# Performance work log

Measured on AMD Instinct MI355X. Metric: run time of the kernel, lower is better.

## Reference

```python
import jax, jax.numpy as jnp
import numpy as np

N, D_HID, D_PROJ = 10000, 256, 256
TAU = 0.5


def setup_inputs() -> dict:
    key = jax.random.key(0)
    ks = jax.random.split(key, 7)
    s = 1.0 / np.sqrt(D_HID)
    return {
        "z1": jax.random.normal(ks[0], (N, D_HID), jnp.float32),
        "z2": jax.random.normal(ks[1], (N, D_HID), jnp.float32),
        "z3": jax.random.normal(ks[2], (N, D_HID), jnp.float32),
        "W1": jax.random.normal(ks[3], (D_PROJ, D_HID), jnp.float32) * s,
        "b1": jnp.zeros((D_PROJ,), jnp.float32),
        "W2": jax.random.normal(ks[4], (D_HID, D_PROJ), jnp.float32) * s,
        "b2": jnp.zeros((D_HID,), jnp.float32),
    }


def _projection(z, W1, b1, W2, b2):
    h = jax.nn.elu(z @ W1.T + b1)
    return h @ W2.T + b2


def _normalize(z, eps=1e-12):
    n = jnp.linalg.norm(z, axis=1, keepdims=True)
    return z / jnp.maximum(n, eps)


def _semi_loss(z1, z2, z3, tau):
    # exp of three NxN cosine-similarity matrices / tau
    intra = jnp.exp(z1 @ z1.T / tau)
    inter = jnp.exp(z1 @ z2.T / tau)
    neg = jnp.exp(z1 @ z3.T / tau)
    denom = (intra.sum(1) + inter.sum(1) + neg.sum(1)
             - jnp.diag(intra) - jnp.diag(inter) - jnp.diag(neg))
    return -jnp.log(jnp.diag(inter) / denom)


def reference(z1, z2, z3, W1, b1, W2, b2):
    p1 = _normalize(_projection(z1, W1, b1, W2, b2))
    p2 = _normalize(_projection(z2, W1, b1, W2, b2))
    p3 = _normalize(_projection(z3, W1, b1, W2, b2))
    l1 = _semi_loss(p1, p2, p3, TAU)
    l2 = _semi_loss(p2, p1, p3, TAU)
    return ((l1 + l2) * 0.5).mean()
```

## Files before the change

kernel.cpp:

```cpp
#include <hip/hip_runtime.h>
#include <hip/hip_bf16.h>
#include <hip/hip_fp8.h>
#include <math.h>

#define AS1 __attribute__((address_space(1)))
#define AS3 __attribute__((address_space(3)))

typedef __bf16 bf16x8 __attribute__((ext_vector_type(8)));
typedef __bf16 bf16x4 __attribute__((ext_vector_type(4)));
typedef float  f32x4  __attribute__((ext_vector_type(4)));
typedef long   longx2 __attribute__((ext_vector_type(2)));

static constexpr int   N_ROWS   = 10000;
static constexpr int   D        = 256;
static constexpr float INV_TAU  = 2.0f;

static constexpr int   T        = 79;
static constexpr int   NP       = T * 128;
static constexpr float PADF     = 112.0f;
static constexpr int   SPR     = 10;
static constexpr int   BPJ     = T * SPR;
static constexpr int   NWGG    = 5 * BPJ;

static constexpr int   PT       = 79;

__device__ __forceinline__ void tile_gemm_128(
    const __bf16* __restrict__ Abase, const __bf16* __restrict__ Bbase,
    char* ldsA, char* ldsB, int tid, f32x4 acc[4][4])
{
  const int l      = tid & 63;
  const int wr     = (tid >> 7) & 1;
  const int wc     = (tid >> 6) & 1;
  const int srow   = tid >> 3;
  const int schunk = tid & 7;
  const int lrow   = l & 15;
  const int lk     = l >> 4;

  for (int kt = 0; kt < 4; ++kt) {
    __syncthreads();
    const int kbase = kt * 64;
#pragma unroll
    for (int rr = 0; rr < 4; ++rr) {
      const int row = rr * 32 + srow;
      const int lc  = schunk ^ (row & 7);
      const __bf16* ga = Abase + (size_t)row * D + kbase + lc * 8;
      const __bf16* gb = Bbase + (size_t)row * D + kbase + lc * 8;
      __builtin_amdgcn_global_load_lds((const AS1 void*)ga,
          (AS3 void*)(ldsA + rr * 4096 + tid * 16), 16, 0, 0);
      __builtin_amdgcn_global_load_lds((const AS1 void*)gb,
          (AS3 void*)(ldsB + rr * 4096 + tid * 16), 16, 0, 0);
    }
    __syncthreads();
#pragma unroll
    for (int ks = 0; ks < 2; ++ks) {
      bf16x8 af[4], bfr[4];
#pragma unroll
      for (int m = 0; m < 4; ++m) {
        const int row = wr * 64 + m * 16 + lrow;
        const int off = row * 128 + ((ks * 64 + lk * 16) ^ ((row & 7) << 4));
        af[m] = *(const bf16x8*)(ldsA + off);
      }
#pragma unroll
      for (int n = 0; n < 4; ++n) {
        const int row = wc * 64 + n * 16 + lrow;
        const int off = row * 128 + ((ks * 64 + lk * 16) ^ ((row & 7) << 4));
        bfr[n] = *(const bf16x8*)(ldsB + off);
      }
#pragma unroll
      for (int m = 0; m < 4; ++m)
#pragma unroll
        for (int n = 0; n < 4; ++n)
          acc[m][n] = __builtin_amdgcn_mfma_f32_16x16x32_bf16(
              af[m], bfr[n], acc[m][n], 0, 0, 0);
    }
  }
}

__global__ __launch_bounds__(256, 3) void gram_kernel(
    const unsigned char* __restrict__ p1, const unsigned char* __restrict__ p2,
    const unsigned char* __restrict__ p3, float* __restrict__ S)
{
  const int bid = blockIdx.x;
  const int job = bid / BPJ;
  const int t0  = bid % BPJ;
  const int r   = t0 / SPR;
  const int s   = t0 % SPR;
  int cstart = s * 8;
  const int cend = min(cstart + 8, T);

  const unsigned char *P, *Q;
  float *Srow, *Scol;
  bool sym = false;
  if (job == 0)      { P = p1; Q = p2; Srow = S + 1 * NP; Scol = S + 3 * NP; }
  else if (job == 1) { P = p1; Q = p3; Srow = S + 2 * NP; Scol = nullptr; }
  else if (job == 2) { P = p2; Q = p3; Srow = S + 5 * NP; Scol = nullptr; }
  else if (job == 3) { P = p1; Q = p1; Srow = S + 0 * NP; Scol = S + 0 * NP;
                       sym = true; cstart = max(cstart, r); }
  else               { P = p2; Q = p2; Srow = S + 4 * NP; Scol = S + 4 * NP;
                       sym = true; cstart = max(cstart, r); }
  const int len = cend - cstart;
  if (len <= 0) return;
  const int nsteps = len * 4;

  __shared__ __align__(16) char lds[49152];
  char* ldsB = lds + 32768;

  const int tid  = threadIdx.x;
  const int l    = tid & 63;
  const int wave = tid >> 6;
  const int wr   = wave >> 1;
  const int wc   = wave & 1;
  const int lrow = l & 15;
  const int lk   = l >> 4;

  int offA[4][4];
#pragma unroll
  for (int m = 0; m < 4; ++m) {
    const int row = wr * 64 + m * 16 + lrow;
    const int swz = (row >> 1) & 7;
#pragma unroll
    for (int kt = 0; kt < 4; ++kt)
      offA[kt][m] = row * 256 + (((kt * 4 + lk) ^ swz) << 4);
  }
  int offB[4];
#pragma unroll
  for (int n = 0; n < 4; ++n) {
    const int row = wc * 64 + n * 16 + lrow;
    offB[n] = row * 64 + ((lk ^ ((row >> 1) & 3)) << 4);
  }

  const unsigned char* Abase = P + (size_t)r * 128 * 256;
#pragma unroll
  for (int j = 0; j < 8; ++j) {
    const int p = tid + j * 256;
    const int row = p >> 4, pc = p & 15;
    __builtin_amdgcn_global_load_lds(
        (const AS1 void*)(Abase + (size_t)row * 256 +
                          ((pc ^ ((row >> 1) & 7)) << 4)),
        (AS3 void*)(lds + p * 16), 16, 0, 0);
  }

  auto stageB = [&](int buf, int i) {
    const int c  = cstart + (i >> 2);
    const int kb = (i & 3) * 64;
    const unsigned char* B0 = Q + (size_t)c * 128 * 256 + kb;
    char* lb = ldsB + buf * 8192;
#pragma unroll
    for (int j = 0; j < 2; ++j) {
      const int p = tid + j * 256;
      const int row = p >> 2, pc = p & 3;
      __builtin_amdgcn_global_load_lds(
          (const AS1 void*)(B0 + (size_t)row * 256 +
                            ((pc ^ ((row >> 1) & 3)) << 4)),
          (AS3 void*)(lb + p * 16), 16, 0, 0);
    }
  };
  stageB(0, 0);

  f32x4 rsum[4];
#pragma unroll
  for (int m = 0; m < 4; ++m)
#pragma unroll
    for (int q = 0; q < 4; ++q) rsum[m][q] = 0.f;

  for (int tt = 0; tt < len; ++tt) {
    f32x4 acc[4][4];
#pragma unroll
    for (int m = 0; m < 4; ++m)
#pragma unroll
      for (int n = 0; n < 4; ++n)
#pragma unroll
        for (int q = 0; q < 4; ++q) acc[m][n][q] = 0.f;

#pragma unroll
    for (int kt = 0; kt < 4; ++kt) {
      const int i = tt * 4 + kt;
      __syncthreads();
      if (i + 1 < nsteps) stageB((i + 1) & 1, i + 1);
      const char* lb = ldsB + (i & 1) * 8192;
      longx2 af[4], bfr[4];
#pragma unroll
      for (int m = 0; m < 4; ++m)
        af[m] = *(const longx2*)(lds + offA[kt][m]);
#pragma unroll
      for (int n = 0; n < 4; ++n)
        bfr[n] = *(const longx2*)(lb + offB[n]);
#pragma unroll
      for (int m = 0; m < 4; ++m)
#pragma unroll
        for (int n = 0; n < 4; ++n)
          acc[m][n] = __builtin_amdgcn_mfma_f32_16x16x32_fp8_fp8(
              af[m][0], bfr[n][0], acc[m][n], 0, 0, 0);
#pragma unroll
      for (int m = 0; m < 4; ++m)
#pragma unroll
        for (int n = 0; n < 4; ++n)
          acc[m][n] = __builtin_amdgcn_mfma_f32_16x16x32_fp8_fp8(
              af[m][1], bfr[n][1], acc[m][n], 0, 0, 0);
    }

    const int c = cstart + tt;
#pragma unroll
    for (int m = 0; m < 4; ++m)
#pragma unroll
      for (int n = 0; n < 4; ++n)
#pragma unroll
        for (int q = 0; q < 4; ++q)
          acc[m][n][q] = __expf(acc[m][n][q] * INV_TAU);

#pragma unroll
    for (int m = 0; m < 4; ++m)
      rsum[m] += acc[m][0] + acc[m][1] + acc[m][2] + acc[m][3];

    const bool docol = Scol && (!sym || c > r);
    if (docol) {
#pragma unroll
      for (int n = 0; n < 4; ++n) {
        float sc = 0.f;
#pragma unroll
        for (int m = 0; m < 4; ++m)
#pragma unroll
          for (int q = 0; q < 4; ++q) sc += acc[m][n][q];
        sc += __shfl_xor(sc, 16, 64);
        sc += __shfl_xor(sc, 32, 64);
        if (l < 16) atomicAdd(&Scol[c * 128 + wc * 64 + n * 16 + l], sc);
      }
    }
  }

#pragma unroll
  for (int m = 0; m < 4; ++m) {
#pragma unroll
    for (int mask = 1; mask < 16; mask <<= 1)
#pragma unroll
      for (int q = 0; q < 4; ++q)
        rsum[m][q] += __shfl_xor(rsum[m][q], mask, 64);
    if ((l & 15) == 0) {
      const int grow = r * 128 + wr * 64 + m * 16 + lk * 4;
#pragma unroll
      for (int q = 0; q < 4; ++q) atomicAdd(&Srow[grow + q], rsum[m][q]);
    }
  }
}

template <int MODE>
__global__ __launch_bounds__(256, 2) void proj_kernel(
    const __bf16* __restrict__ A, const __bf16* __restrict__ B,
    const float* __restrict__ bias, void* __restrict__ out)
{
  const int r = blockIdx.x, c = blockIdx.y;
  __shared__ __align__(16) char lds[32768];
  f32x4 acc[4][4];
#pragma unroll
  for (int m = 0; m < 4; ++m)
#pragma unroll
    for (int n = 0; n < 4; ++n)
#pragma unroll
      for (int q = 0; q < 4; ++q) acc[m][n][q] = 0.f;

  tile_gemm_128(A + (size_t)r * 128 * D, B + (size_t)c * 128 * D,
                lds, lds + 16384, threadIdx.x, acc);

  const int tid = threadIdx.x, l = tid & 63;
  const int wr = (tid >> 7) & 1, wc = (tid >> 6) & 1;
#pragma unroll
  for (int n = 0; n < 4; ++n) {
    const int gcol = c * 128 + wc * 64 + n * 16 + (l & 15);
    const float bn = bias[gcol];
#pragma unroll
    for (int m = 0; m < 4; ++m) {
#pragma unroll
      for (int q = 0; q < 4; ++q) {
        const int grow = r * 128 + wr * 64 + m * 16 + (l >> 4) * 4 + q;
        float v = acc[m][n][q] + bn;
        if (MODE == 0) {
          float o = v > 0.f ? v : (__expf(v) - 1.f);
          ((__bf16*)out)[(size_t)grow * D + gcol] = (__bf16)o;
        } else {
          ((float*)out)[(size_t)grow * D + gcol] = v;
        }
      }
    }
  }
}

__global__ void cast_kernel(const float* __restrict__ src,
                            __bf16* __restrict__ dst, int n)
{
  int idx = (blockIdx.x * blockDim.x + threadIdx.x) * 4;
  const int stride = gridDim.x * blockDim.x * 4;
  for (; idx < n; idx += stride) {
    const float4 v = *(const float4*)(src + idx);
    bf16x4 o;
    o[0] = (__bf16)v.x; o[1] = (__bf16)v.y;
    o[2] = (__bf16)v.z; o[3] = (__bf16)v.w;
    *(bf16x4*)(dst + idx) = o;
  }
}

__global__ void norm_kernel(const float* __restrict__ praw,
                            __bf16* __restrict__ p,
                            unsigned char* __restrict__ pf)
{
  const int row = blockIdx.x * 4 + (threadIdx.x >> 6);
  const int l = threadIdx.x & 63;
  const size_t base = (size_t)row * D + l * 4;
  if (row < N_ROWS) {
    const float4 v = *(const float4*)(praw + base);
    float ss = v.x * v.x + v.y * v.y + v.z * v.z + v.w * v.w;
#pragma unroll
    for (int mask = 1; mask < 64; mask <<= 1) ss += __shfl_xor(ss, mask, 64);
    const float inv = 1.0f / fmaxf(sqrtf(ss), 1e-12f);
    const float f0 = v.x * inv, f1 = v.y * inv, f2 = v.z * inv, f3 = v.w * inv;
    bf16x4 o;
    o[0] = (__bf16)f0; o[1] = (__bf16)f1; o[2] = (__bf16)f2; o[3] = (__bf16)f3;
    *(bf16x4*)(p + base) = o;
    const unsigned int b0 = __hip_fp8_e4m3(f0).__x;
    const unsigned int b1 = __hip_fp8_e4m3(f1).__x;
    const unsigned int b2 = __hip_fp8_e4m3(f2).__x;
    const unsigned int b3 = __hip_fp8_e4m3(f3).__x;
    *(unsigned int*)(pf + base) = b0 | (b1 << 8) | (b2 << 16) | (b3 << 24);
  } else {
    bf16x4 o;
    o[0] = o[1] = o[2] = o[3] = (__bf16)0.0f;
    *(bf16x4*)(p + base) = o;
    *(unsigned int*)(pf + base) = 0u;
  }
}

__global__ void diag_kernel(const __bf16* __restrict__ p1,
                            const __bf16* __restrict__ p2,
                            const __bf16* __restrict__ p3,
                            float* __restrict__ dg)
{
  const int row = blockIdx.x * 4 + (threadIdx.x >> 6);
  const int l = threadIdx.x & 63;
  if (row >= N_ROWS) return;
  const size_t base = (size_t)row * D + l * 4;
  const bf16x4 a = *(const bf16x4*)(p1 + base);
  const bf16x4 b = *(const bf16x4*)(p2 + base);
  const bf16x4 e = *(const bf16x4*)(p3 + base);
  float d11 = 0, d22 = 0, d12 = 0, d13 = 0, d23 = 0;
#pragma unroll
  for (int q = 0; q < 4; ++q) {
    const float fa = (float)a[q], fb = (float)b[q], fe = (float)e[q];
    d11 += fa * fa; d22 += fb * fb; d12 += fa * fb;
    d13 += fa * fe; d23 += fb * fe;
  }
#pragma unroll
  for (int mask = 1; mask < 64; mask <<= 1) {
    d11 += __shfl_xor(d11, mask, 64);
    d22 += __shfl_xor(d22, mask, 64);
    d12 += __shfl_xor(d12, mask, 64);
    d13 += __shfl_xor(d13, mask, 64);
    d23 += __shfl_xor(d23, mask, 64);
  }
  if (l == 0) {
    dg[0 * NP + row] = __expf(d11 * INV_TAU);
    dg[1 * NP + row] = __expf(d22 * INV_TAU);
    dg[2 * NP + row] = __expf(d12 * INV_TAU);
    dg[3 * NP + row] = __expf(d13 * INV_TAU);
    dg[4 * NP + row] = __expf(d23 * INV_TAU);
  }
}

__global__ void loss_kernel(const float* __restrict__ S,
                            const float* __restrict__ dg,
                            float* __restrict__ out)
{
  float local = 0.f;
  for (int i = blockIdx.x * blockDim.x + threadIdx.x; i < N_ROWS;
       i += gridDim.x * blockDim.x) {
    const float s11 = S[0 * NP + i] - PADF;
    const float s12 = S[1 * NP + i] - PADF;
    const float s13 = S[2 * NP + i] - PADF;
    const float s21 = S[3 * NP + i] - PADF;
    const float s22 = S[4 * NP + i] - PADF;
    const float s23 = S[5 * NP + i] - PADF;
    const float d11 = dg[0 * NP + i], d22 = dg[1 * NP + i];
    const float d12 = dg[2 * NP + i], d13 = dg[3 * NP + i];
    const float d23 = dg[4 * NP + i];
    const float den1 = s11 + s12 + s13 - d11 - d12 - d13;
    const float den2 = s22 + s21 + s23 - d22 - d12 - d23;
    local += 0.5f * (__logf(den1) + __logf(den2)) - __logf(d12);
  }
#pragma unroll
  for (int mask = 1; mask < 64; mask <<= 1) local += __shfl_xor(local, mask, 64);
  __shared__ float wsum[4];
  if ((threadIdx.x & 63) == 0) wsum[threadIdx.x >> 6] = local;
  __syncthreads();
  if (threadIdx.x == 0) {
    const float t = wsum[0] + wsum[1] + wsum[2] + wsum[3];
    atomicAdd(out, t * (1.0f / (float)N_ROWS));
  }
}

extern "C" void kernel_launch(void* const* d_in, const int* in_sizes, int n_in,
                              void* d_out, int out_size, void* d_ws,
                              size_t ws_size, hipStream_t stream)
{
  const float* z[3] = {(const float*)d_in[0], (const float*)d_in[1],
                       (const float*)d_in[2]};
  const float* W1 = (const float*)d_in[3];
  const float* b1 = (const float*)d_in[4];
  const float* W2 = (const float*)d_in[5];
  const float* b2 = (const float*)d_in[6];

  char* ws = (char*)d_ws;
  size_t off = 0;
  auto alloc = [&](size_t bytes) -> char* {
    char* p = ws + off;
    off += (bytes + 511) & ~(size_t)511;
    return p;
  };
  __bf16* pB[3];
  unsigned char* pF[3];
  for (int m = 0; m < 3; ++m) pB[m] = (__bf16*)alloc((size_t)NP * D * 2);
  for (int m = 0; m < 3; ++m) pF[m] = (unsigned char*)alloc((size_t)NP * D);
  __bf16* w1b  = (__bf16*)alloc((size_t)D * D * 2);
  __bf16* w2b  = (__bf16*)alloc((size_t)D * D * 2);
  __bf16* zb   = (__bf16*)alloc((size_t)NP * D * 2);
  __bf16* hB   = (__bf16*)alloc((size_t)NP * D * 2);
  float*  praw = (float*) alloc((size_t)NP * D * 4);
  float*  Sv   = (float*) alloc((size_t)6 * NP * 4);
  float*  dg   = (float*) alloc((size_t)5 * NP * 4);

  hipMemsetAsync(Sv, 0, (size_t)6 * NP * 4, stream);
  hipMemsetAsync(d_out, 0, sizeof(float), stream);

  cast_kernel<<<64, 256, 0, stream>>>(W1, w1b, D * D);
  cast_kernel<<<64, 256, 0, stream>>>(W2, w2b, D * D);

  for (int m = 0; m < 3; ++m) {
    cast_kernel<<<2500, 256, 0, stream>>>(z[m], zb, N_ROWS * D);
    dim3 g(PT, 2);
    proj_kernel<0><<<g, 256, 0, stream>>>(zb, w1b, b1, (void*)hB);
    proj_kernel<1><<<g, 256, 0, stream>>>(hB, w2b, b2, (void*)praw);
    norm_kernel<<<NP / 4, 256, 0, stream>>>(praw, pB[m], pF[m]);
  }

  gram_kernel<<<NWGG, 256, 0, stream>>>(pF[0], pF[1], pF[2], Sv);
  diag_kernel<<<2500, 256, 0, stream>>>(pB[0], pB[1], pB[2], dg);
  loss_kernel<<<64, 256, 0, stream>>>(Sv, dg, (float*)d_out);
}
```

Baseline: 248.8 us.

## Batch the three projection pipelines into single launches and fold tau into fp8 scaling

The per-view loop of cast, two projection GEMMs and normalization becomes one launch per stage, using a z grid dimension over the three views whenever the workspace is large enough. This removes launch overhead and fills more of the GPU, since each projection grid previously had only 158 workgroups. The 1/tau factor is also folded into the fp8 operands by scaling each by sqrt(2) before quantization, which drops a multiply per element in the gram exp. The costs are three times more workspace and a slightly different fp8 quantization range.

```diff
diff --git a/kernel.cpp b/kernel.cpp
--- a/kernel.cpp
+++ b/kernel.cpp
@@ -13,7 +13,6 @@
 
 static constexpr int   N_ROWS   = 10000;
 static constexpr int   D        = 256;
-static constexpr float INV_TAU  = 2.0f;
 
 static constexpr int   T        = 79;
 static constexpr int   NP       = T * 128;
@@ -206,7 +205,7 @@
       for (int n = 0; n < 4; ++n)
 #pragma unroll
         for (int q = 0; q < 4; ++q)
-          acc[m][n][q] = __expf(acc[m][n][q] * INV_TAU);
+          acc[m][n][q] = __expf(acc[m][n][q]);
 
 #pragma unroll
     for (int m = 0; m < 4; ++m)
@@ -246,9 +245,12 @@
 template <int MODE>
 __global__ __launch_bounds__(256, 2) void proj_kernel(
     const __bf16* __restrict__ A, const __bf16* __restrict__ B,
-    const float* __restrict__ bias, void* __restrict__ out)
+    const float* __restrict__ bias, void* __restrict__ out,
+    size_t strideA, size_t strideOut)
 {
   const int r = blockIdx.x, c = blockIdx.y;
+  const size_t zo = (size_t)blockIdx.z;
+  A += zo * strideA;
   __shared__ __align__(16) char lds[32768];
   f32x4 acc[4][4];
 #pragma unroll
@@ -275,9 +277,9 @@
         float v = acc[m][n][q] + bn;
         if (MODE == 0) {
           float o = v > 0.f ? v : (__expf(v) - 1.f);
-          ((__bf16*)out)[(size_t)grow * D + gcol] = (__bf16)o;
+          ((__bf16*)out)[zo * strideOut + (size_t)grow * D + gcol] = (__bf16)o;
         } else {
-          ((float*)out)[(size_t)grow * D + gcol] = v;
+          ((float*)out)[zo * strideOut + (size_t)grow * D + gcol] = v;
         }
       }
     }
@@ -298,13 +300,33 @@
   }
 }
 
+__global__ void cast3_kernel(const float* __restrict__ z0,
+                             const float* __restrict__ z1,
+                             const float* __restrict__ z2,
+                             __bf16* __restrict__ dst, size_t strideElems)
+{
+  const int n = N_ROWS * D;
+  int idx = (blockIdx.x * blockDim.x + threadIdx.x) * 4;
+  const int stride = gridDim.x * blockDim.x * 4;
+  for (; idx < 3 * n; idx += stride) {
+    const int m = idx / n, e = idx - m * n;
+    const float* src = (m == 0) ? z0 : (m == 1) ? z1 : z2;
+    const float4 v = *(const float4*)(src + e);
+    bf16x4 o;
+    o[0] = (__bf16)v.x; o[1] = (__bf16)v.y;
+    o[2] = (__bf16)v.z; o[3] = (__bf16)v.w;
+    *(bf16x4*)(dst + m * strideElems + e) = o;
+  }
+}
+
 __global__ void norm_kernel(const float* __restrict__ praw,
                             __bf16* __restrict__ p,
                             unsigned char* __restrict__ pf)
 {
+  const size_t mo = (size_t)blockIdx.y * NP * D;
   const int row = blockIdx.x * 4 + (threadIdx.x >> 6);
   const int l = threadIdx.x & 63;
-  const size_t base = (size_t)row * D + l * 4;
+  const size_t base = mo + (size_t)row * D + l * 4;
   if (row < N_ROWS) {
     const float4 v = *(const float4*)(praw + base);
     float ss = v.x * v.x + v.y * v.y + v.z * v.z + v.w * v.w;
@@ -315,10 +337,11 @@
     bf16x4 o;
     o[0] = (__bf16)f0; o[1] = (__bf16)f1; o[2] = (__bf16)f2; o[3] = (__bf16)f3;
     *(bf16x4*)(p + base) = o;
-    const unsigned int b0 = __hip_fp8_e4m3(f0).__x;
-    const unsigned int b1 = __hip_fp8_e4m3(f1).__x;
-    const unsigned int b2 = __hip_fp8_e4m3(f2).__x;
-    const unsigned int b3 = __hip_fp8_e4m3(f3).__x;
+    const float SC = 1.41421356237f;
+    const unsigned int b0 = __hip_fp8_e4m3(f0 * SC).__x;
+    const unsigned int b1 = __hip_fp8_e4m3(f1 * SC).__x;
+    const unsigned int b2 = __hip_fp8_e4m3(f2 * SC).__x;
+    const unsigned int b3 = __hip_fp8_e4m3(f3 * SC).__x;
     *(unsigned int*)(pf + base) = b0 | (b1 << 8) | (b2 << 16) | (b3 << 24);
   } else {
     bf16x4 o;
@@ -356,11 +379,11 @@
     d23 += __shfl_xor(d23, mask, 64);
   }
   if (l == 0) {
-    dg[0 * NP + row] = __expf(d11 * INV_TAU);
-    dg[1 * NP + row] = __expf(d22 * INV_TAU);
-    dg[2 * NP + row] = __expf(d12 * INV_TAU);
-    dg[3 * NP + row] = __expf(d13 * INV_TAU);
-    dg[4 * NP + row] = __expf(d23 * INV_TAU);
+    dg[0 * NP + row] = __expf(d11 * 2.0f);
+    dg[1 * NP + row] = __expf(d22 * 2.0f);
+    dg[2 * NP + row] = __expf(d12 * 2.0f);
+    dg[3 * NP + row] = __expf(d13 * 2.0f);
+    dg[4 * NP + row] = __expf(d23 * 2.0f);
   }
 }
 
@@ -413,33 +436,50 @@
     off += (bytes + 511) & ~(size_t)511;
     return p;
   };
-  __bf16* pB[3];
-  unsigned char* pF[3];
-  for (int m = 0; m < 3; ++m) pB[m] = (__bf16*)alloc((size_t)NP * D * 2);
-  for (int m = 0; m < 3; ++m) pF[m] = (unsigned char*)alloc((size_t)NP * D);
+  const size_t PE = (size_t)NP * D;
+  __bf16*        pB3 = (__bf16*)alloc(3 * PE * 2);
+  unsigned char* pF3 = (unsigned char*)alloc(3 * PE);
   __bf16* w1b  = (__bf16*)alloc((size_t)D * D * 2);
   __bf16* w2b  = (__bf16*)alloc((size_t)D * D * 2);
-  __bf16* zb   = (__bf16*)alloc((size_t)NP * D * 2);
-  __bf16* hB   = (__bf16*)alloc((size_t)NP * D * 2);
-  float*  praw = (float*) alloc((size_t)NP * D * 4);
   float*  Sv   = (float*) alloc((size_t)6 * NP * 4);
   float*  dg   = (float*) alloc((size_t)5 * NP * 4);
 
+  const size_t common = off;
+  const size_t batched_need = common + 3 * ((PE * 2 + 511 & ~511ull) +
+                              (PE * 2 + 511 & ~511ull)) + 3 * (PE * 4) + 4096;
+  const bool batched = ws_size >= batched_need;
+
   hipMemsetAsync(Sv, 0, (size_t)6 * NP * 4, stream);
   hipMemsetAsync(d_out, 0, sizeof(float), stream);
 
   cast_kernel<<<64, 256, 0, stream>>>(W1, w1b, D * D);
   cast_kernel<<<64, 256, 0, stream>>>(W2, w2b, D * D);
 
-  for (int m = 0; m < 3; ++m) {
-    cast_kernel<<<2500, 256, 0, stream>>>(z[m], zb, N_ROWS * D);
-    dim3 g(PT, 2);
-    proj_kernel<0><<<g, 256, 0, stream>>>(zb, w1b, b1, (void*)hB);
-    proj_kernel<1><<<g, 256, 0, stream>>>(hB, w2b, b2, (void*)praw);
-    norm_kernel<<<NP / 4, 256, 0, stream>>>(praw, pB[m], pF[m]);
-  }
-
-  gram_kernel<<<NWGG, 256, 0, stream>>>(pF[0], pF[1], pF[2], Sv);
-  diag_kernel<<<2500, 256, 0, stream>>>(pB[0], pB[1], pB[2], dg);
+  if (batched) {
+    __bf16* zb3   = (__bf16*)alloc(3 * PE * 2);
+    __bf16* hB3   = (__bf16*)alloc(3 * PE * 2);
+    float*  praw3 = (float*) alloc(3 * PE * 4);
+    cast3_kernel<<<2048, 256, 0, stream>>>(z[0], z[1], z[2], zb3, PE);
+    dim3 g(PT, 2, 3);
+    proj_kernel<0><<<g, 256, 0, stream>>>(zb3, w1b, b1, (void*)hB3, PE, PE);
+    proj_kernel<1><<<g, 256, 0, stream>>>(hB3, w2b, b2, (void*)praw3, PE, PE);
+    dim3 gn(NP / 4, 3);
+    norm_kernel<<<gn, 256, 0, stream>>>(praw3, pB3, pF3);
+  } else {
+    __bf16* zb   = (__bf16*)alloc(PE * 2);
+    __bf16* hB   = (__bf16*)alloc(PE * 2);
+    float*  praw = (float*) alloc(PE * 4);
+    for (int m = 0; m < 3; ++m) {
+      cast_kernel<<<2500, 256, 0, stream>>>(z[m], zb, N_ROWS * D);
+      dim3 g(PT, 2, 1);
+      proj_kernel<0><<<g, 256, 0, stream>>>(zb, w1b, b1, (void*)hB, 0, 0);
+      proj_kernel<1><<<g, 256, 0, stream>>>(hB, w2b, b2, (void*)praw, 0, 0);
+      dim3 gn(NP / 4, 1);
+      norm_kernel<<<gn, 256, 0, stream>>>(praw, pB3 + m * PE, pF3 + m * PE);
+    }
+  }
+
+  gram_kernel<<<NWGG, 256, 0, stream>>>(pF3, pF3 + PE, pF3 + 2 * PE, Sv);
+  diag_kernel<<<2500, 256, 0, stream>>>(pB3, pB3 + PE, pB3 + 2 * PE, dg);
   loss_kernel<<<64, 256, 0, stream>>>(Sv, dg, (float*)d_out);
 }
```

Measured after the change: 211.3 us. 15.1% less time.
